# Optimization experiments

Hardware: AMD Instinct MI355X
Metric: run time of the kernel (lower is better)

Reference implementation:

```python
import jax, jax.numpy as jnp
import numpy as np

DIM = 768
HEADS = 12
HEAD_DIM = DIM // HEADS
EPS = 1e-12  # torch F.normalize eps


def setup_inputs() -> dict:
    key = jax.random.key(0)
    k1, k2, k3 = jax.random.split(key, 3)
    x = jax.random.normal(k1, (8, 4096, DIM), dtype=jnp.float32)
    # qkv: Linear(dim, 3*dim, bias=False); proj: Linear(dim, dim) with bias
    s = 1.0 / np.sqrt(DIM)
    w_qkv = jax.random.uniform(k2, (3 * DIM, DIM), dtype=jnp.float32, minval=-s, maxval=s)
    w_proj = jax.random.uniform(k3, (DIM, DIM), dtype=jnp.float32, minval=-s, maxval=s)
    b_proj = jnp.zeros((DIM,), dtype=jnp.float32)
    return {"x": x, "w_qkv": w_qkv, "w_proj": w_proj, "b_proj": b_proj}


def _l1_normalize(t):
    # normalize over token axis N (axis=-2), matching F.normalize(p=1, dim=-2)
    denom = jnp.maximum(jnp.sum(jnp.abs(t), axis=-2, keepdims=True), EPS)
    return t / denom


def reference(x, w_qkv, w_proj, b_proj):
    B, N, C = x.shape
    hd = C // HEADS
    qkv = x @ w_qkv.T  # [B, N, 3C]
    qkv = qkv.reshape(B, N, 3, HEADS, hd).transpose(2, 0, 3, 1, 4)  # [3, B, H, N, hd]
    q, k, v = qkv[0], qkv[1], qkv[2]
    q = _l1_normalize(q)
    k = _l1_normalize(k)
    if N < hd:
        out = jnp.einsum('bhnd,bhmd,bhme->bhne', q, k, v)
    else:
        kv = jnp.einsum('bhnd,bhne->bhde', k, v)  # [B, H, hd, hd]
        out = jnp.einsum('bhnd,bhde->bhne', q, kv)  # [B, H, N, hd]
    out = out.transpose(0, 2, 1, 3).reshape(B, N, C)
    return out @ w_proj.T + b_proj
```

## Files before the change

### kernel.cpp

```cpp
#include <hip/hip_runtime.h>
#include <cstddef>
#include <cstdint>

#define DIMC   768
#define HEADS  12
#define HD     64
#define BATCH  8
#define SEQ    4096
#define MTOK   (BATCH*SEQ)
#define THREEC (3*DIMC)
#define BHN    (BATCH*HEADS)
#define NCHUNK 8
#define CHTOK  (SEQ/NCHUNK)
#define EPSN   1e-12f
#define KT     (DIMC/32)
#define TILE_U16 1024
#define ROWTILE_U16 (KT*TILE_U16)

typedef unsigned short u16;
typedef unsigned int   u32;
typedef __attribute__((ext_vector_type(8))) short short8;
typedef __attribute__((ext_vector_type(4))) float f32x4;

__device__ inline u16 bf16_rne(float f) {
  u32 u = __float_as_uint(f);
  u32 r = u + 0x7fffu + ((u >> 16) & 1u);
  return (u16)(r >> 16);
}

__device__ inline u32 cvt_pk_bf16(float a, float b) {
  u32 r;
  asm("v_cvt_pk_bf16_f32 %0, %1, %2" : "=v"(r) : "v"(a), "v"(b));
  return r;
}

__global__ __launch_bounds__(256)
void split_tiles(const float* __restrict__ in, u16* __restrict__ outp,
                 int nrowtiles) {
  const int l = threadIdx.x & 63;
  const int ntiles = nrowtiles * KT;
  for (int gw = (blockIdx.x * 256 + threadIdx.x) >> 6; gw < ntiles;
       gw += (gridDim.x * 256) >> 6) {
    const int rt = gw / KT, kt = gw % KT;
    const float* src = in + (size_t)(rt * 16 + (l & 15)) * DIMC + kt * 32 + (l >> 4) * 8;
    float4 x0 = *(const float4*)src;
    float4 x1 = *(const float4*)(src + 4);
    float xs[8] = {x0.x, x0.y, x0.z, x0.w, x1.x, x1.y, x1.z, x1.w};
    u32 hw[4], lw[4];
    #pragma unroll
    for (int i = 0; i < 4; ++i) {
      u16 h0 = bf16_rne(xs[2*i]);
      u16 h1 = bf16_rne(xs[2*i+1]);
      float r0 = xs[2*i]   - __uint_as_float(((u32)h0) << 16);
      float r1 = xs[2*i+1] - __uint_as_float(((u32)h1) << 16);
      u16 l0 = bf16_rne(r0);
      u16 l1 = bf16_rne(r1);
      hw[i] = (u32)h0 | ((u32)h1 << 16);
      lw[i] = (u32)l0 | ((u32)l1 << 16);
    }
    u16* tb = outp + (size_t)gw * TILE_U16;
    *(uint4*)(tb + l * 8)       = make_uint4(hw[0], hw[1], hw[2], hw[3]);
    *(uint4*)(tb + 512 + l * 8) = make_uint4(lw[0], lw[1], lw[2], lw[3]);
  }
}

__global__ __launch_bounds__(256)
void split_tiles_t(const float* __restrict__ in, u16* __restrict__ outp,
                   int nrowtiles, int ld) {
  const int l = threadIdx.x & 63;
  const int ntiles = nrowtiles * KT;
  for (int gw = (blockIdx.x * 256 + threadIdx.x) >> 6; gw < ntiles;
       gw += (gridDim.x * 256) >> 6) {
    const int rt = gw / KT, kt = gw % KT;
    const int m = rt * 16 + (l & 15);
    const int k0 = kt * 32 + (l >> 4) * 8;
    float xs[8];
    #pragma unroll
    for (int j = 0; j < 8; ++j) xs[j] = in[(size_t)(k0 + j) * ld + m];
    u32 hw[4], lw[4];
    #pragma unroll
    for (int i = 0; i < 4; ++i) {
      u16 h0 = bf16_rne(xs[2*i]);
      u16 h1 = bf16_rne(xs[2*i+1]);
      float r0 = xs[2*i]   - __uint_as_float(((u32)h0) << 16);
      float r1 = xs[2*i+1] - __uint_as_float(((u32)h1) << 16);
      u16 l0 = bf16_rne(r0);
      u16 l1 = bf16_rne(r1);
      hw[i] = (u32)h0 | ((u32)h1 << 16);
      lw[i] = (u32)l0 | ((u32)l1 << 16);
    }
    u16* tb = outp + (size_t)gw * TILE_U16;
    *(uint4*)(tb + l * 8)       = make_uint4(hw[0], hw[1], hw[2], hw[3]);
    *(uint4*)(tb + 512 + l * 8) = make_uint4(lw[0], lw[1], lw[2], lw[3]);
  }
}

__global__ __launch_bounds__(256, 3)
void qkv_stage1(const u16* __restrict__ xc, const u16* __restrict__ wc,
                float* __restrict__ kvp, float* __restrict__ dqp,
                float* __restrict__ dkp) {
  const int bid = blockIdx.x;
  const int h = bid % HEADS;
  const int bc = bid / HEADS;
  const int b = bc >> 3, chunk = bc & 7;
  const int bh = b * HEADS + h;
  const int si = bh * NCHUNK + chunk;

  const int tid = threadIdx.x;
  const int w = tid >> 6, l = tid & 63;
  const int lr16 = l & 15, cg = l >> 4;

  __shared__ __align__(16) unsigned char smem[33792];
  u16* lds16 = (u16*)smem;
  float* red = (float*)smem;

  f32x4 kvacc[4] = {(f32x4){0,0,0,0},(f32x4){0,0,0,0},(f32x4){0,0,0,0},(f32x4){0,0,0,0}};
  float dsum_q = 0.f, dsum_k = 0.f;

  const u16* wbase[3];
  #pragma unroll
  for (int ot = 0; ot < 3; ++ot) {
    const int grow = ot * DIMC + h * HD + w * 16;
    wbase[ot] = wc + (size_t)(grow >> 4) * ROWTILE_U16 + (l << 3);
  }
  const int atile0 = (b * SEQ + chunk * CHTOK) >> 4;

  for (int sub = 0; sub < 8; ++sub) {
    const u16* abase[4];
    #pragma unroll
    for (int tt = 0; tt < 4; ++tt)
      abase[tt] = xc + (size_t)(atile0 + sub * 4 + tt) * ROWTILE_U16 + (l << 3);

    f32x4 acc[4][3];
    #pragma unroll
    for (int tt = 0; tt < 4; ++tt)
      #pragma unroll
      for (int ot = 0; ot < 3; ++ot)
        acc[tt][ot] = (f32x4){0.f, 0.f, 0.f, 0.f};

    for (int kt = 0; kt < KT; ++kt) {
      const int off = kt * TILE_U16;
      short8 bh_[3], bl_[3];
      #pragma unroll
      for (int ot = 0; ot < 3; ++ot) {
        bh_[ot] = *(const short8*)(wbase[ot] + off);
        bl_[ot] = *(const short8*)(wbase[ot] + off + 512);
      }
      #pragma unroll
      for (int tt = 0; tt < 4; ++tt) {
        short8 ah = *(const short8*)(abase[tt] + off);
        short8 al = *(const short8*)(abase[tt] + off + 512);
        #pragma unroll
        for (int ot = 0; ot < 3; ++ot) {
          acc[tt][ot] = __builtin_amdgcn_mfma_f32_16x16x32_bf16(ah, bh_[ot], acc[tt][ot], 0, 0, 0);
          acc[tt][ot] = __builtin_amdgcn_mfma_f32_16x16x32_bf16(ah, bl_[ot], acc[tt][ot], 0, 0, 0);
          acc[tt][ot] = __builtin_amdgcn_mfma_f32_16x16x32_bf16(al, bh_[ot], acc[tt][ot], 0, 0, 0);
        }
      }
    }
    __syncthreads();
    #pragma unroll
    for (int tt = 0; tt < 4; ++tt) {
      dsum_q += fabsf(acc[tt][0][0]);
      dsum_q += fabsf(acc[tt][0][1]);
      dsum_q += fabsf(acc[tt][0][2]);
      dsum_q += fabsf(acc[tt][0][3]);
    }
    #pragma unroll
    for (int sec = 1; sec < 3; ++sec) {
      const int region = (sec == 1) ? 0 : 8192;
      #pragma unroll
      for (int tt = 0; tt < 4; ++tt) {
        const float v0 = acc[tt][sec][0], v1 = acc[tt][sec][1];
        const float v2 = acc[tt][sec][2], v3 = acc[tt][sec][3];
        if (sec == 1) {
          dsum_k += fabsf(v0);
          dsum_k += fabsf(v1);
          dsum_k += fabsf(v2);
          dsum_k += fabsf(v3);
        }
        const u32 ph01 = cvt_pk_bf16(v0, v1);
        const u32 ph23 = cvt_pk_bf16(v2, v3);
        const float r0 = v0 - __uint_as_float(ph01 << 16);
        const float r1 = v1 - __uint_as_float(ph01 & 0xffff0000u);
        const float r2 = v2 - __uint_as_float(ph23 << 16);
        const float r3 = v3 - __uint_as_float(ph23 & 0xffff0000u);
        const u32 pl01 = cvt_pk_bf16(r0, r1);
        const u32 pl23 = cvt_pk_bf16(r2, r3);
        const int pos = region + (w * 2 + (tt >> 1)) * TILE_U16 +
                        ((lr16 | (((tt * 2 + (cg >> 1)) & 3) << 4)) << 3) +
                        ((cg & 1) << 2);
        *(uint2*)(lds16 + pos)       = make_uint2(ph01, ph23);
        *(uint2*)(lds16 + pos + 512) = make_uint2(pl01, pl23);
      }
    }
    __syncthreads();
    {
      const u16* At = lds16 + w * 2 * TILE_U16;
      const u16* Bt = lds16 + 8192;
      #pragma unroll
      for (int t2 = 0; t2 < 2; ++t2) {
        short8 kah = *(const short8*)(At + t2 * TILE_U16 + (l << 3));
        short8 kal = *(const short8*)(At + t2 * TILE_U16 + 512 + (l << 3));
        #pragma unroll
        for (int et = 0; et < 4; ++et) {
          short8 vbh = *(const short8*)(Bt + (et * 2 + t2) * TILE_U16 + (l << 3));
          short8 vbl = *(const short8*)(Bt + (et * 2 + t2) * TILE_U16 + 512 + (l << 3));
          kvacc[et] = __builtin_amdgcn_mfma_f32_16x16x32_bf16(kah, vbh, kvacc[et], 0, 0, 0);
          kvacc[et] = __builtin_amdgcn_mfma_f32_16x16x32_bf16(kah, vbl, kvacc[et], 0, 0, 0);
          kvacc[et] = __builtin_amdgcn_mfma_f32_16x16x32_bf16(kal, vbh, kvacc[et], 0, 0, 0);
        }
      }
    }
  }
  float* ob = kvp + (size_t)si * (HD * HD);
  #pragma unroll
  for (int et = 0; et < 4; ++et)
    #pragma unroll
    for (int r = 0; r < 4; ++r)
      ob[(w * 16 + cg * 4 + r) * HD + et * 16 + lr16] = kvacc[et][r];
  __syncthreads();
  red[(w * 16 + lr16) * 4 + cg]       = dsum_q;
  red[256 + (w * 16 + lr16) * 4 + cg] = dsum_k;
  __syncthreads();
  if (tid < 64) {
    dqp[(size_t)si * HD + tid] = red[tid*4] + red[tid*4+1] + red[tid*4+2] + red[tid*4+3];
  } else if (tid < 128) {
    const int d = tid - 64;
    dkp[(size_t)si * HD + d] = red[256 + d*4] + red[256 + d*4+1] + red[256 + d*4+2] + red[256 + d*4+3];
  }
}

__global__ __launch_bounds__(256)
void kv_reduce(const float* __restrict__ kvp, const float* __restrict__ dqp,
               const float* __restrict__ dkp, float* __restrict__ kvs) {
  const int bh = blockIdx.x;
  const int tid = threadIdx.x;
  __shared__ float dqL[64], dkL[64];
  if (tid < 64) {
    float s = 0.f;
    #pragma unroll
    for (int c = 0; c < NCHUNK; ++c) s += dqp[((size_t)bh * NCHUNK + c) * HD + tid];
    dqL[tid] = fmaxf(s, EPSN);
  } else if (tid < 128) {
    const int d = tid - 64;
    float s = 0.f;
    #pragma unroll
    for (int c = 0; c < NCHUNK; ++c) s += dkp[((size_t)bh * NCHUNK + c) * HD + d];
    dkL[d] = fmaxf(s, EPSN);
  }
  __syncthreads();
  #pragma unroll
  for (int i = 0; i < 16; ++i) {
    const int idx = i * 256 + tid;
    const int d = idx >> 6;
    float s = 0.f;
    #pragma unroll
    for (int c = 0; c < NCHUNK; ++c)
      s += kvp[((size_t)bh * NCHUNK + c) * (HD * HD) + idx];
    kvs[(size_t)bh * (HD * HD) + idx] = s / (dqL[d] * dkL[d]);
  }
}

__global__ __launch_bounds__(256)
void w2_kernel(const float* __restrict__ kvs, const float* __restrict__ w_proj,
               float* __restrict__ W2T) {
  const int bh = blockIdx.x;
  const int b = bh / HEADS, h = bh % HEADS;
  const int c0 = blockIdx.y * 128;
  const int tid = threadIdx.x;
  const int tx = tid & 15, ty = tid >> 4;
  __shared__ float KVe[64][68];
  __shared__ float Wp[64][132];
  #pragma unroll
  for (int i = 0; i < 4; ++i) {
    const int idx = i * 256 + tid;
    const int d  = idx >> 4;
    const int e4 = (idx & 15) << 2;
    float4 v4 = *(const float4*)&kvs[(size_t)bh * (HD*HD) + (size_t)d * HD + e4];
    KVe[e4+0][d] = v4.x; KVe[e4+1][d] = v4.y;
    KVe[e4+2][d] = v4.z; KVe[e4+3][d] = v4.w;
  }
  {
    const int c = tid >> 1, half = tid & 1;
    #pragma unroll
    for (int j = 0; j < 8; ++j) {
      const int e = half * 32 + j * 4;
      float4 v4 = *(const float4*)&w_proj[(size_t)(c0 + c) * DIMC + h * HD + e];
      Wp[e+0][c] = v4.x; Wp[e+1][c] = v4.y; Wp[e+2][c] = v4.z; Wp[e+3][c] = v4.w;
    }
  }
  __syncthreads();
  float acc[4][8] = {};
  for (int e = 0; e < 64; ++e) {
    float4 a4 = *(const float4*)&KVe[e][ty << 2];
    float4 b0 = *(const float4*)&Wp[e][tx << 3];
    float4 b1 = *(const float4*)&Wp[e][(tx << 3) + 4];
    float ar[4] = {a4.x, a4.y, a4.z, a4.w};
    float br[8] = {b0.x,b0.y,b0.z,b0.w,b1.x,b1.y,b1.z,b1.w};
    #pragma unroll
    for (int i = 0; i < 4; ++i)
      #pragma unroll
      for (int j = 0; j < 8; ++j)
        acc[i][j] = fmaf(ar[i], br[j], acc[i][j]);
  }
  float* W2Tb = W2T + (size_t)b * DIMC * DIMC;
  #pragma unroll
  for (int j = 0; j < 8; ++j)
    *(float4*)&W2Tb[(size_t)(c0 + (tx << 3) + j) * DIMC + h * HD + (ty << 2)] =
        make_float4(acc[0][j], acc[1][j], acc[2][j], acc[3][j]);
}

__global__ __launch_bounds__(256)
void w3t_mfma(const u16* __restrict__ w2c, const u16* __restrict__ wqt,
              float* __restrict__ W3T) {
  const int tid = threadIdx.x;
  const int w = tid >> 6, l = tid & 63;
  const int lr16 = l & 15, cg = l >> 4;
  const int cx = blockIdx.x, my = blockIdx.y, b = blockIdx.z;

  const u16* wbase[3];
  #pragma unroll
  for (int ot = 0; ot < 3; ++ot)
    wbase[ot] = wqt + (size_t)(my * 12 + w * 3 + ot) * ROWTILE_U16 + (l << 3);
  const u16* abase[4];
  #pragma unroll
  for (int tt = 0; tt < 4; ++tt)
    abase[tt] = w2c + (size_t)(b * 48 + cx * 4 + tt) * ROWTILE_U16 + (l << 3);

  f32x4 acc[4][3];
  #pragma unroll
  for (int tt = 0; tt < 4; ++tt)
    #pragma unroll
    for (int ot = 0; ot < 3; ++ot)
      acc[tt][ot] = (f32x4){0.f, 0.f, 0.f, 0.f};

  for (int kt = 0; kt < KT; ++kt) {
    const int off = kt * TILE_U16;
    short8 bh_[3], bl_[3];
    #pragma unroll
    for (int ot = 0; ot < 3; ++ot) {
      bh_[ot] = *(const short8*)(wbase[ot] + off);
      bl_[ot] = *(const short8*)(wbase[ot] + off + 512);
    }
    #pragma unroll
    for (int tt = 0; tt < 4; ++tt) {
      short8 ah = *(const short8*)(abase[tt] + off);
      short8 al = *(const short8*)(abase[tt] + off + 512);
      #pragma unroll
      for (int ot = 0; ot < 3; ++ot) {
        acc[tt][ot] = __builtin_amdgcn_mfma_f32_16x16x32_bf16(ah, bh_[ot], acc[tt][ot], 0, 0, 0);
        acc[tt][ot] = __builtin_amdgcn_mfma_f32_16x16x32_bf16(ah, bl_[ot], acc[tt][ot], 0, 0, 0);
        acc[tt][ot] = __builtin_amdgcn_mfma_f32_16x16x32_bf16(al, bh_[ot], acc[tt][ot], 0, 0, 0);
      }
    }
  }
  float* Wb = W3T + (size_t)b * DIMC * DIMC;
  #pragma unroll
  for (int ot = 0; ot < 3; ++ot) {
    const int col = my * 192 + w * 48 + ot * 16 + lr16;
    #pragma unroll
    for (int tt = 0; tt < 4; ++tt) {
      const int row0 = cx * 64 + tt * 16 + cg * 4;
      #pragma unroll
      for (int r = 0; r < 4; ++r)
        Wb[(size_t)(row0 + r) * DIMC + col] = acc[tt][ot][r];
    }
  }
}

__global__ __launch_bounds__(256, 3)
void final_gemm_mfma(const u16* __restrict__ xc, const u16* __restrict__ w3c,
                     const float* __restrict__ bias, float* __restrict__ out) {
  const int tid = threadIdx.x;
  const int w = tid >> 6, l = tid & 63;
  const int lr16 = l & 15, cg = l >> 4;
  const int ntile = blockIdx.x;
  const int c0 = blockIdx.y * 192;
  const int b = ntile >> 6;
  const int colbase0 = c0 + w * 48;

  const u16* wbase[3];
  #pragma unroll
  for (int ot = 0; ot < 3; ++ot) {
    const int c = colbase0 + ot * 16;
    wbase[ot] = w3c + (size_t)(b * (DIMC/16) + (c >> 4)) * ROWTILE_U16 + (l << 3);
  }
  const u16* abase[4];
  #pragma unroll
  for (int tt = 0; tt < 4; ++tt)
    abase[tt] = xc + (size_t)(ntile * 4 + tt) * ROWTILE_U16 + (l << 3);

  f32x4 acc[4][3];
  #pragma unroll
  for (int tt = 0; tt < 4; ++tt)
    #pragma unroll
    for (int ot = 0; ot < 3; ++ot)
      acc[tt][ot] = (f32x4){0.f, 0.f, 0.f, 0.f};

  for (int kt = 0; kt < KT; ++kt) {
    const int off = kt * TILE_U16;
    short8 bh_[3], bl_[3];
    #pragma unroll
    for (int ot = 0; ot < 3; ++ot) {
      bh_[ot] = *(const short8*)(wbase[ot] + off);
      bl_[ot] = *(const short8*)(wbase[ot] + off + 512);
    }
    #pragma unroll
    for (int tt = 0; tt < 4; ++tt) {
      short8 ah = *(const short8*)(abase[tt] + off);
      short8 al = *(const short8*)(abase[tt] + off + 512);
      #pragma unroll
      for (int ot = 0; ot < 3; ++ot) {
        acc[tt][ot] = __builtin_amdgcn_mfma_f32_16x16x32_bf16(ah, bh_[ot], acc[tt][ot], 0, 0, 0);
        acc[tt][ot] = __builtin_amdgcn_mfma_f32_16x16x32_bf16(ah, bl_[ot], acc[tt][ot], 0, 0, 0);
        acc[tt][ot] = __builtin_amdgcn_mfma_f32_16x16x32_bf16(al, bh_[ot], acc[tt][ot], 0, 0, 0);
      }
    }
  }
  #pragma unroll
  for (int ot = 0; ot < 3; ++ot) {
    const int col = colbase0 + ot * 16 + lr16;
    const float bv = bias[col];
    #pragma unroll
    for (int tt = 0; tt < 4; ++tt) {
      const size_t row0 = (size_t)ntile * 64 + tt * 16 + cg * 4;
      #pragma unroll
      for (int r = 0; r < 4; ++r)
        out[(row0 + r) * DIMC + col] = acc[tt][ot][r] + bv;
    }
  }
}

extern "C" void kernel_launch(void* const* d_in, const int* in_sizes, int n_in,
                              void* d_out, int out_size, void* d_ws, size_t ws_size,
                              hipStream_t stream) {
  const float* x      = (const float*)d_in[0];
  const float* w_qkv  = (const float*)d_in[1];
  const float* w_proj = (const float*)d_in[2];
  const float* b_proj = (const float*)d_in[3];
  float* out = (float*)d_out;
  float* ws  = (float*)d_ws;

  const size_t KVP_SZ = (size_t)BHN * NCHUNK * HD * HD;
  const size_t DQP_SZ = (size_t)BHN * NCHUNK * HD;
  const size_t KVS_SZ = (size_t)BHN * HD * HD;
  const size_t W_SZ   = (size_t)BATCH * DIMC * DIMC;
  const size_t XC_U16  = (size_t)(MTOK/16) * ROWTILE_U16;
  const size_t WC_U16  = (size_t)(THREEC/16) * ROWTILE_U16;
  const size_t WQT_U16 = (size_t)(DIMC/16) * ROWTILE_U16;
  const size_t W2C_U16 = (size_t)(BATCH*DIMC/16) * ROWTILE_U16;
  const size_t W3C_U16 = (size_t)(BATCH*DIMC/16) * ROWTILE_U16;
  float* kvp  = ws;
  float* dqp  = kvp + KVP_SZ;
  float* dkp  = dqp + DQP_SZ;
  float* kvs  = dkp + DQP_SZ;
  float* WBUF = kvs + KVS_SZ;
  u16*   xc   = (u16*)(WBUF + W_SZ);
  u16*   wc   = xc + XC_U16;
  u16*   wqt  = wc + WC_U16;
  u16*   w2c  = wqt + WQT_U16;
  u16*   w3c  = w2c + W2C_U16;
  const size_t need_bytes =
      (KVP_SZ + 2*DQP_SZ + KVS_SZ + W_SZ) * sizeof(float) +
      (XC_U16 + WC_U16 + WQT_U16 + W2C_U16 + W3C_U16) * sizeof(u16);
  if (ws_size < need_bytes) return;

  const dim3 blk(256);
  split_tiles<<<dim3((MTOK/16) * KT / 4), blk, 0, stream>>>(x, xc, MTOK/16);
  split_tiles<<<dim3((THREEC/16) * KT / 4), blk, 0, stream>>>(w_qkv, wc, THREEC/16);
  split_tiles_t<<<dim3((DIMC/16) * KT / 4), blk, 0, stream>>>(w_qkv, wqt, DIMC/16, DIMC);
  qkv_stage1<<<dim3(BHN * NCHUNK), blk, 0, stream>>>(xc, wc, kvp, dqp, dkp);
  kv_reduce<<<dim3(BHN), blk, 0, stream>>>(kvp, dqp, dkp, kvs);
  w2_kernel<<<dim3(BHN, DIMC/128), blk, 0, stream>>>(kvs, w_proj, WBUF);
  split_tiles<<<dim3((BATCH*DIMC/16) * KT / 4), blk, 0, stream>>>(WBUF, w2c, BATCH*DIMC/16);
  w3t_mfma<<<dim3(DIMC/64, DIMC/192, BATCH), blk, 0, stream>>>(w2c, wqt, WBUF);
  split_tiles<<<dim3((BATCH*DIMC/16) * KT / 4), blk, 0, stream>>>(WBUF, w3c, BATCH*DIMC/16);
  final_gemm_mfma<<<dim3(MTOK/64, DIMC/192), blk, 0, stream>>>(xc, w3c, b_proj, out);
}
```

Baseline: 555.3 us.

## Stage activation tiles through double-buffered LDS instead of per-wave global loads

```diff
diff --git a/kernel.cpp b/kernel.cpp
--- a/kernel.cpp
+++ b/kernel.cpp
@@ -126,10 +126,16 @@
   const int atile0 = (b * SEQ + chunk * CHTOK) >> 4;
 
   for (int sub = 0; sub < 8; ++sub) {
-    const u16* abase[4];
-    #pragma unroll
-    for (int tt = 0; tt < 4; ++tt)
-      abase[tt] = xc + (size_t)(atile0 + sub * 4 + tt) * ROWTILE_U16 + (l << 3);
+    const u16* asub = xc + (size_t)(atile0 + sub * 4) * ROWTILE_U16;
+    __syncthreads();
+    {
+      const u16* g = asub + (size_t)w * ROWTILE_U16 + (l << 3);
+      uint4 s0 = *(const uint4*)g;
+      uint4 s1 = *(const uint4*)(g + 512);
+      *(uint4*)(lds16 + w * 1024 + (l << 3))       = s0;
+      *(uint4*)(lds16 + w * 1024 + 512 + (l << 3)) = s1;
+    }
+    __syncthreads();
 
     f32x4 acc[4][3];
     #pragma unroll
@@ -139,6 +145,14 @@
         acc[tt][ot] = (f32x4){0.f, 0.f, 0.f, 0.f};
 
     for (int kt = 0; kt < KT; ++kt) {
+      const int cur = (kt & 1) << 12;
+      const int nxt = cur ^ 4096;
+      uint4 s0, s1;
+      if (kt + 1 < KT) {
+        const u16* g = asub + (size_t)w * ROWTILE_U16 + (kt + 1) * TILE_U16 + (l << 3);
+        s0 = *(const uint4*)g;
+        s1 = *(const uint4*)(g + 512);
+      }
       const int off = kt * TILE_U16;
       short8 bh_[3], bl_[3];
       #pragma unroll
@@ -148,8 +162,8 @@
       }
       #pragma unroll
       for (int tt = 0; tt < 4; ++tt) {
-        short8 ah = *(const short8*)(abase[tt] + off);
-        short8 al = *(const short8*)(abase[tt] + off + 512);
+        short8 ah = *(const short8*)(lds16 + cur + tt * 1024 + (l << 3));
+        short8 al = *(const short8*)(lds16 + cur + tt * 1024 + 512 + (l << 3));
         #pragma unroll
         for (int ot = 0; ot < 3; ++ot) {
           acc[tt][ot] = __builtin_amdgcn_mfma_f32_16x16x32_bf16(ah, bh_[ot], acc[tt][ot], 0, 0, 0);
@@ -157,8 +171,12 @@
           acc[tt][ot] = __builtin_amdgcn_mfma_f32_16x16x32_bf16(al, bh_[ot], acc[tt][ot], 0, 0, 0);
         }
       }
-    }
-    __syncthreads();
+      if (kt + 1 < KT) {
+        *(uint4*)(lds16 + nxt + w * 1024 + (l << 3))       = s0;
+        *(uint4*)(lds16 + nxt + w * 1024 + 512 + (l << 3)) = s1;
+      }
+      __syncthreads();
+    }
     #pragma unroll
     for (int tt = 0; tt < 4; ++tt) {
       dsum_q += fabsf(acc[tt][0][0]);
```

New measurement: 547.5 us. Within noise of the previous version (-1.4%).
